# Performance work log

Measured on AMD Instinct MI355X. Metric: run time of the kernel, lower is better.

The kernel has to match this reference:

```python
import jax, jax.numpy as jnp
import numpy as np
import jax.lax as lax

B, S, E, H = 8, 4096, 1024, 128
TAU = 1.0
MIN_K = 32

def setup_inputs() -> dict:
    key = jax.random.key(0)
    k0, k1, k2, k3 = jax.random.split(key, 4)
    token_embeddings = jax.random.normal(k0, (B, S, E), dtype=jnp.float32)
    w1 = jax.random.normal(k1, (E, H), dtype=jnp.float32) * (1.0 / np.sqrt(E))
    b1 = jnp.zeros((H,), dtype=jnp.float32)
    w2 = jax.random.normal(k2, (H, 1), dtype=jnp.float32) * (1.0 / np.sqrt(H))
    b2 = jnp.zeros((1,), dtype=jnp.float32)
    # uniform noise for Gumbel, same bounds as the original module
    u = jax.random.uniform(k3, (B, S), minval=1e-08, maxval=1.0 - 1e-08, dtype=jnp.float32)
    return {"token_embeddings": token_embeddings, "w1": w1, "b1": b1, "w2": w2, "b2": b2, "u": u}

def reference(token_embeddings, w1, b1, w2, b2, u):
    # scorer MLP: Dense(H) -> relu -> Dense(1), squeeze -> [B, S]
    h = jax.nn.relu(jnp.einsum('bse,eh->bsh', token_embeddings, w1) + b1)
    importance_logits = (jnp.einsum('bsh,ho->bso', h, w2) + b2)[..., 0]  # [B, S]

    # expected_k (value_function is None): soft count of kept tokens
    expected_k = jax.nn.sigmoid(importance_logits).sum(axis=-1)  # [B]
    k = jnp.clip(expected_k.astype(jnp.int32), MIN_K, None)      # [B]

    # Gumbel-softmax top-k, hard=True
    gumbel = -jnp.log(-jnp.log(u))
    soft_mask = jax.nn.softmax((importance_logits + gumbel) / TAU, axis=-1)  # [B, S]

    # hard mask: 1.0 at the top-k[i] positions of soft_mask per row.
    # Equivalent to the original argsort + while_loop scatter: positions with
    # descending-sort rank < k[i] get 1.0.
    order = jnp.argsort(-soft_mask, axis=-1)          # [B, S] descending order
    ranks = jnp.argsort(order, axis=-1)               # rank of each position
    hard_mask = (ranks < k[:, None]).astype(soft_mask.dtype)

    selection_mask = lax.stop_gradient(hard_mask - soft_mask) + soft_mask
    filtered_embeddings = token_embeddings * selection_mask[..., None]
    return filtered_embeddings, selection_mask, expected_k
```

## Files before the change

kernel.cpp:

```cpp
#include <hip/hip_runtime.h>
#include <hip/hip_bf16.h>
#include <math.h>

#define B_ 8
#define S_ 4096
#define E_ 1024
#define H_ 128
#define MIN_K 32
#define OUT_MASK_OFF (B_*S_*E_)
#define OUT_EK_OFF   (B_*S_*E_ + B_*S_)

#define LOGITS_OFF 0
#define SOFT_OFF   131072
#define CNT_OFF    262144
#define KROW_OFF   393216
#define WB_OFF     393248

typedef __attribute__((ext_vector_type(8))) short   frag8;
typedef __attribute__((ext_vector_type(4))) float   fragc;

static __device__ __forceinline__ unsigned short bf16_rne(float f) {
  unsigned u = __float_as_uint(f);
  unsigned r = u + 0x7FFF + ((u >> 16) & 1);
  return (unsigned short)(r >> 16);
}
static __device__ __forceinline__ float bf16_to_f32(unsigned short h) {
  return __uint_as_float(((unsigned)h) << 16);
}

__global__ __launch_bounds__(256) void prep_w_kernel(
    const float* __restrict__ w1, unsigned short* __restrict__ wb)
{
  int id = blockIdx.x * 256 + threadIdx.x;
  int k  = id >> 5;
  int n4 = id & 31;
  float4 w = *(const float4*)(w1 + k * H_ + n4 * 4);
  int t  = k >> 5;
  int kp = k & 31;
#pragma unroll
  for (int e = 0; e < 4; ++e) {
    float f = (e == 0) ? w.x : (e == 1) ? w.y : (e == 2) ? w.z : w.w;
    unsigned short hi = bf16_rne(f);
    unsigned short lo = bf16_rne(f - bf16_to_f32(hi));
    int n = n4 * 4 + e;
    wb[t * 8192 +        n * 32 + kp] = hi;
    wb[t * 8192 + 4096 + n * 32 + kp] = lo;
  }
}

#define KT 32
#define NTILES (E_ / KT)
#define XS 40

__global__ __launch_bounds__(512, 2) void scorer_kernel(
    const float* __restrict__ x,
    const unsigned short* __restrict__ wb,
    const float* __restrict__ b1, const float* __restrict__ w2,
    const float* __restrict__ b2, float* __restrict__ logits)
{
  __shared__ unsigned short as_hi[2][128 * XS];
  __shared__ unsigned short as_lo[2][128 * XS];
  __shared__ unsigned short bs_hi[2][128 * XS];
  __shared__ unsigned short bs_lo[2][128 * XS];
  __shared__ float part[2][128];

  const int tid  = threadIdx.x;
  const int wv   = tid >> 6;
  const int lane = tid & 63;
  const int l15  = lane & 15;
  const int quad = lane >> 4;
  const int mg   = wv >> 1;
  const int ng   = wv & 1;
  const int m0   = blockIdx.x * 128;

  const int r = tid >> 2, p = tid & 3;
  const float* __restrict__ xsrc = x + (size_t)(m0 + r) * E_ + p * 8;
  const unsigned short* __restrict__ bsrc = wb + tid * 16;
  const int bplane = tid >> 8;
  const int boff   = ((tid >> 1) & 127) * XS + (tid & 1) * 16;
  const int aoff   = r * XS + p * 8;

  fragc acc[2][4];
#pragma unroll
  for (int mt = 0; mt < 2; ++mt)
#pragma unroll
    for (int nt = 0; nt < 4; ++nt)
      acc[mt][nt] = (fragc)(0.f);

  float4 a0 = *(const float4*)(xsrc);
  float4 a1 = *(const float4*)(xsrc + 4);
  uint4  q0 = *(const uint4*)(bsrc);
  uint4  q1 = *(const uint4*)(bsrc + 8);
  {
    frag8 h8, l8;
    float f[8] = {a0.x, a0.y, a0.z, a0.w, a1.x, a1.y, a1.z, a1.w};
#pragma unroll
    for (int e = 0; e < 8; ++e) {
      unsigned short hi = bf16_rne(f[e]);
      h8[e] = (short)hi; l8[e] = (short)bf16_rne(f[e] - bf16_to_f32(hi));
    }
    *(frag8*)&as_hi[0][aoff] = h8;
    *(frag8*)&as_lo[0][aoff] = l8;
    unsigned short* bd = bplane ? &bs_lo[0][boff] : &bs_hi[0][boff];
    *(uint4*)(bd) = q0;
    *(uint4*)(bd + 8) = q1;
  }
  __syncthreads();

#pragma unroll 1
  for (int t = 0; t < NTILES; ++t) {
    const int buf = t & 1;
    const bool more = (t + 1 < NTILES);

    float4 na0, na1; uint4 nq0, nq1;
    if (more) {
      na0 = *(const float4*)(xsrc + (t + 1) * KT);
      na1 = *(const float4*)(xsrc + (t + 1) * KT + 4);
      nq0 = *(const uint4*)(bsrc + (t + 1) * 8192);
      nq1 = *(const uint4*)(bsrc + (t + 1) * 8192 + 8);
    }

    frag8 ah[2], al[2], bh[4], bl[4];
#pragma unroll
    for (int mt = 0; mt < 2; ++mt) {
      int a = (mg * 32 + mt * 16 + l15) * XS + quad * 8;
      ah[mt] = *(const frag8*)&as_hi[buf][a];
      al[mt] = *(const frag8*)&as_lo[buf][a];
    }
#pragma unroll
    for (int nt = 0; nt < 4; ++nt) {
      int a = (ng * 64 + nt * 16 + l15) * XS + quad * 8;
      bh[nt] = *(const frag8*)&bs_hi[buf][a];
      bl[nt] = *(const frag8*)&bs_lo[buf][a];
    }

#pragma unroll
    for (int mt = 0; mt < 2; ++mt)
#pragma unroll
      for (int nt = 0; nt < 4; ++nt) {
        acc[mt][nt] = __builtin_amdgcn_mfma_f32_16x16x32_bf16(ah[mt], bh[nt], acc[mt][nt], 0, 0, 0);
        acc[mt][nt] = __builtin_amdgcn_mfma_f32_16x16x32_bf16(ah[mt], bl[nt], acc[mt][nt], 0, 0, 0);
        acc[mt][nt] = __builtin_amdgcn_mfma_f32_16x16x32_bf16(al[mt], bh[nt], acc[mt][nt], 0, 0, 0);
      }

    if (more) {
      frag8 h8, l8;
      float f[8] = {na0.x, na0.y, na0.z, na0.w, na1.x, na1.y, na1.z, na1.w};
#pragma unroll
      for (int e = 0; e < 8; ++e) {
        unsigned short hi = bf16_rne(f[e]);
        h8[e] = (short)hi; l8[e] = (short)bf16_rne(f[e] - bf16_to_f32(hi));
      }
      *(frag8*)&as_hi[buf ^ 1][aoff] = h8;
      *(frag8*)&as_lo[buf ^ 1][aoff] = l8;
      unsigned short* bd = bplane ? &bs_lo[buf ^ 1][boff] : &bs_hi[buf ^ 1][boff];
      *(uint4*)(bd) = nq0;
      *(uint4*)(bd + 8) = nq1;
    }
    __syncthreads();
  }

  float b1v[4], w2v[4];
#pragma unroll
  for (int nt = 0; nt < 4; ++nt) {
    int n = ng * 64 + nt * 16 + l15;
    b1v[nt] = b1[n]; w2v[nt] = w2[n];
  }
  float v[2][4];
#pragma unroll
  for (int mt = 0; mt < 2; ++mt)
#pragma unroll
    for (int reg = 0; reg < 4; ++reg) {
      float pacc = 0.f;
#pragma unroll
      for (int nt = 0; nt < 4; ++nt) {
        float h = acc[mt][nt][reg] + b1v[nt];
        h = h > 0.f ? h : 0.f;
        pacc = fmaf(h, w2v[nt], pacc);
      }
      v[mt][reg] = pacc;
    }
#pragma unroll
  for (int mask = 1; mask < 16; mask <<= 1)
#pragma unroll
    for (int mt = 0; mt < 2; ++mt)
#pragma unroll
      for (int reg = 0; reg < 4; ++reg)
        v[mt][reg] += __shfl_xor(v[mt][reg], mask);

  if (l15 == 0) {
#pragma unroll
    for (int mt = 0; mt < 2; ++mt)
#pragma unroll
      for (int reg = 0; reg < 4; ++reg)
        part[ng][mg * 32 + mt * 16 + quad * 4 + reg] = v[mt][reg];
  }
  __syncthreads();
  if (tid < 128)
    logits[m0 + tid] = (part[0][tid] + part[1][tid]) + b2[0];
}

__global__ __launch_bounds__(1024) void row_kernel(
    const float* __restrict__ logits, const float* __restrict__ u,
    float* __restrict__ soft, int* __restrict__ krow, float* __restrict__ ek_out)
{
  const int b = blockIdx.x;
  const int t = threadIdx.x;
  const float* Lrow = logits + b * S_;
  const float* urow = u + b * S_;

  __shared__ double red[1024];
  __shared__ float  redf[1024];

  float z[4];
  double psig = 0.0;
  float zmax = -INFINITY;
#pragma unroll
  for (int i = 0; i < 4; ++i) {
    int j = t + i * 1024;
    float L = Lrow[j];
    float g = -logf(-logf(urow[j]));
    z[i] = L + g;
    psig += (double)(1.f / (1.f + expf(-L)));
    zmax = fmaxf(zmax, z[i]);
  }
  red[t] = psig; redf[t] = zmax;
  __syncthreads();
  for (int s2 = 512; s2 > 0; s2 >>= 1) {
    if (t < s2) { red[t] += red[t + s2]; redf[t] = fmaxf(redf[t], redf[t + s2]); }
    __syncthreads();
  }
  __shared__ float m_sh; __shared__ double ek_sh;
  if (t == 0) { m_sh = redf[0]; ek_sh = red[0]; }
  __syncthreads();
  float m = m_sh;

  float e[4];
  double pexp = 0.0;
#pragma unroll
  for (int i = 0; i < 4; ++i) { e[i] = expf(z[i] - m); pexp += (double)e[i]; }
  red[t] = pexp;
  __syncthreads();
  for (int s2 = 512; s2 > 0; s2 >>= 1) {
    if (t < s2) red[t] += red[t + s2];
    __syncthreads();
  }
  __shared__ float den_sh;
  if (t == 0) den_sh = (float)red[0];
  __syncthreads();
  float den = den_sh;
#pragma unroll
  for (int i = 0; i < 4; ++i) soft[b * S_ + t + i * 1024] = e[i] / den;

  if (t == 0) {
    float ekf = (float)ek_sh;
    int k = (int)ekf;
    if (k < MIN_K) k = MIN_K;
    krow[b] = k;
    ek_out[b] = ekf;
  }
}

__global__ __launch_bounds__(256) void rank_kernel(
    const float* __restrict__ soft, int* __restrict__ counts)
{
  __shared__ float4 sjs[256];
  const int b  = blockIdx.z;
  const int ic = blockIdx.x;
  const int jc = blockIdx.y;
  const int tid = threadIdx.x;
  const float* row = soft + b * S_;

  sjs[tid] = ((const float4*)row)[jc * 256 + tid];
  const int i = ic * 256 + tid;
  const float si = row[i];
  __syncthreads();

  int cnt = 0;
  const int jbase = jc * 1024;
  for (int j4 = 0; j4 < 256; ++j4) {
    float4 vv = sjs[j4];
    int j = jbase + j4 * 4;
    cnt += (vv.x > si) || (vv.x == si && (j + 0) < i);
    cnt += (vv.y > si) || (vv.y == si && (j + 1) < i);
    cnt += (vv.z > si) || (vv.z == si && (j + 2) < i);
    cnt += (vv.w > si) || (vv.w == si && (j + 3) < i);
  }
  atomicAdd(&counts[b * S_ + i], cnt);
}

__global__ __launch_bounds__(256) void filter_kernel(
    const float* __restrict__ x, const float* __restrict__ soft,
    const int* __restrict__ counts, const int* __restrict__ krow,
    float* __restrict__ out, float* __restrict__ mask_out)
{
  const int token = blockIdx.x;
  const int b = token >> 12;
  const float s = soft[token];
  const float h = (counts[token] < krow[b]) ? 1.f : 0.f;
  const float sel = (h - s) + s;

  size_t base = (size_t)token * (E_ / 4) + threadIdx.x;
  float4 v = ((const float4*)x)[base];
  v.x *= sel; v.y *= sel; v.z *= sel; v.w *= sel;
  ((float4*)out)[base] = v;
  if (threadIdx.x == 0) mask_out[token] = sel;
}

extern "C" void kernel_launch(void* const* d_in, const int* in_sizes, int n_in,
                              void* d_out, int out_size, void* d_ws, size_t ws_size,
                              hipStream_t stream) {
  const float* x  = (const float*)d_in[0];
  const float* w1 = (const float*)d_in[1];
  const float* b1 = (const float*)d_in[2];
  const float* w2 = (const float*)d_in[3];
  const float* b2 = (const float*)d_in[4];
  const float* u  = (const float*)d_in[5];

  float* out = (float*)d_out;
  float* out_filt = out;
  float* out_mask = out + OUT_MASK_OFF;
  float* out_ek   = out + OUT_EK_OFF;

  char* ws = (char*)d_ws;
  float*          ws_logits = (float*)(ws + LOGITS_OFF);
  float*          ws_soft   = (float*)(ws + SOFT_OFF);
  int*            ws_cnt    = (int*)(ws + CNT_OFF);
  int*            ws_krow   = (int*)(ws + KROW_OFF);
  unsigned short* ws_wb     = (unsigned short*)(ws + WB_OFF);

  hipMemsetAsync(ws_cnt, 0, B_ * S_ * sizeof(int), stream);
  prep_w_kernel<<<dim3(128), dim3(256), 0, stream>>>(w1, ws_wb);
  scorer_kernel<<<dim3(B_ * S_ / 128), dim3(512), 0, stream>>>(
      x, ws_wb, b1, w2, b2, ws_logits);
  row_kernel<<<dim3(B_), dim3(1024), 0, stream>>>(ws_logits, u, ws_soft, ws_krow, out_ek);
  rank_kernel<<<dim3(16, 4, 8), dim3(256), 0, stream>>>(ws_soft, ws_cnt);
  filter_kernel<<<dim3(B_ * S_), dim3(256), 0, stream>>>(
      x, ws_soft, ws_cnt, ws_krow, out_filt, out_mask);
}
```

Before: 313.8 us.

## Stage raw fp32 activations in LDS and deepen global prefetch to two tiles

The scorer GEMM loop now stores raw fp32 activation tiles in shared memory and does the bf16 hi/lo split at fragment-load time, not before the LDS store. The loop is unrolled by two with register double-buffering, so global loads run two K-tiles ahead, and sched_barriers keep the loads issued before compute. This aims to hide global memory latency better and shorten the store path. In exchange, the split conversion is now repeated per wave that reads the same A rows (both N-groups), and register pressure rises from holding two prefetch stages.

```diff
diff --git a/kernel.cpp b/kernel.cpp
--- a/kernel.cpp
+++ b/kernel.cpp
@@ -50,7 +50,43 @@
 
 #define KT 32
 #define NTILES (E_ / KT)
+#define AS 36
 #define XS 40
+
+#define ISSUE_LOADS(Sa0, Sa1, Sq0, Sq1, T)                  \
+    Sa0 = *(const float4*)(xsrc + (T) * KT);                \
+    Sa1 = *(const float4*)(xsrc + (T) * KT + 4);            \
+    Sq0 = *(const uint4*)(bsrc + (T) * 8192);               \
+    Sq1 = *(const uint4*)(bsrc + (T) * 8192 + 8);
+
+#define WRITE_STAGE(BUF, Sa0, Sa1, Sq0, Sq1) {              \
+    *(float4*)&as_f[BUF][aoff]     = Sa0;                   \
+    *(float4*)&as_f[BUF][aoff + 4] = Sa1;                   \
+    unsigned short* bd_ = bplane ? &bs_lo[BUF][boff]        \
+                                 : &bs_hi[BUF][boff];       \
+    *(uint4*)(bd_)     = Sq0;                               \
+    *(uint4*)(bd_ + 8) = Sq1; }
+
+#define COMPUTE(BUF) {                                                        \
+    frag8 ah[2], al[2], bh[4], bl[4];                                         \
+    _Pragma("unroll") for (int mt = 0; mt < 2; ++mt) {                        \
+      int a_ = (mg * 32 + mt * 16 + l15) * AS + quad * 8;                     \
+      float4 f0_ = *(const float4*)&as_f[BUF][a_];                            \
+      float4 f1_ = *(const float4*)&as_f[BUF][a_ + 4];                        \
+      float ff_[8] = {f0_.x, f0_.y, f0_.z, f0_.w, f1_.x, f1_.y, f1_.z, f1_.w};\
+      _Pragma("unroll") for (int e = 0; e < 8; ++e) {                         \
+        unsigned short hi_ = bf16_rne(ff_[e]);                                \
+        ah[mt][e] = (short)hi_;                                               \
+        al[mt][e] = (short)bf16_rne(ff_[e] - bf16_to_f32(hi_)); } }           \
+    _Pragma("unroll") for (int nt = 0; nt < 4; ++nt) {                        \
+      int a_ = (ng * 64 + nt * 16 + l15) * XS + quad * 8;                     \
+      bh[nt] = *(const frag8*)&bs_hi[BUF][a_];                                \
+      bl[nt] = *(const frag8*)&bs_lo[BUF][a_]; }                              \
+    _Pragma("unroll") for (int mt = 0; mt < 2; ++mt)                          \
+      _Pragma("unroll") for (int nt = 0; nt < 4; ++nt) {                      \
+        acc[mt][nt] = __builtin_amdgcn_mfma_f32_16x16x32_bf16(ah[mt], bh[nt], acc[mt][nt], 0, 0, 0); \
+        acc[mt][nt] = __builtin_amdgcn_mfma_f32_16x16x32_bf16(ah[mt], bl[nt], acc[mt][nt], 0, 0, 0); \
+        acc[mt][nt] = __builtin_amdgcn_mfma_f32_16x16x32_bf16(al[mt], bh[nt], acc[mt][nt], 0, 0, 0); } }
 
 __global__ __launch_bounds__(512, 2) void scorer_kernel(
     const float* __restrict__ x,
@@ -58,8 +94,7 @@
     const float* __restrict__ b1, const float* __restrict__ w2,
     const float* __restrict__ b2, float* __restrict__ logits)
 {
-  __shared__ unsigned short as_hi[2][128 * XS];
-  __shared__ unsigned short as_lo[2][128 * XS];
+  __shared__ float          as_f[2][128 * AS];
   __shared__ unsigned short bs_hi[2][128 * XS];
   __shared__ unsigned short bs_lo[2][128 * XS];
   __shared__ float part[2][128];
@@ -78,7 +113,7 @@
   const unsigned short* __restrict__ bsrc = wb + tid * 16;
   const int bplane = tid >> 8;
   const int boff   = ((tid >> 1) & 127) * XS + (tid & 1) * 16;
-  const int aoff   = r * XS + p * 8;
+  const int aoff   = r * AS + p * 8;
 
   fragc acc[2][4];
 #pragma unroll
@@ -87,76 +122,25 @@
     for (int nt = 0; nt < 4; ++nt)
       acc[mt][nt] = (fragc)(0.f);
 
-  float4 a0 = *(const float4*)(xsrc);
-  float4 a1 = *(const float4*)(xsrc + 4);
-  uint4  q0 = *(const uint4*)(bsrc);
-  uint4  q1 = *(const uint4*)(bsrc + 8);
-  {
-    frag8 h8, l8;
-    float f[8] = {a0.x, a0.y, a0.z, a0.w, a1.x, a1.y, a1.z, a1.w};
-#pragma unroll
-    for (int e = 0; e < 8; ++e) {
-      unsigned short hi = bf16_rne(f[e]);
-      h8[e] = (short)hi; l8[e] = (short)bf16_rne(f[e] - bf16_to_f32(hi));
-    }
-    *(frag8*)&as_hi[0][aoff] = h8;
-    *(frag8*)&as_lo[0][aoff] = l8;
-    unsigned short* bd = bplane ? &bs_lo[0][boff] : &bs_hi[0][boff];
-    *(uint4*)(bd) = q0;
-    *(uint4*)(bd + 8) = q1;
-  }
-  __syncthreads();
-
-#pragma unroll 1
-  for (int t = 0; t < NTILES; ++t) {
-    const int buf = t & 1;
-    const bool more = (t + 1 < NTILES);
-
-    float4 na0, na1; uint4 nq0, nq1;
-    if (more) {
-      na0 = *(const float4*)(xsrc + (t + 1) * KT);
-      na1 = *(const float4*)(xsrc + (t + 1) * KT + 4);
-      nq0 = *(const uint4*)(bsrc + (t + 1) * 8192);
-      nq1 = *(const uint4*)(bsrc + (t + 1) * 8192 + 8);
-    }
-
-    frag8 ah[2], al[2], bh[4], bl[4];
-#pragma unroll
-    for (int mt = 0; mt < 2; ++mt) {
-      int a = (mg * 32 + mt * 16 + l15) * XS + quad * 8;
-      ah[mt] = *(const frag8*)&as_hi[buf][a];
-      al[mt] = *(const frag8*)&as_lo[buf][a];
-    }
-#pragma unroll
-    for (int nt = 0; nt < 4; ++nt) {
-      int a = (ng * 64 + nt * 16 + l15) * XS + quad * 8;
-      bh[nt] = *(const frag8*)&bs_hi[buf][a];
-      bl[nt] = *(const frag8*)&bs_lo[buf][a];
-    }
-
-#pragma unroll
-    for (int mt = 0; mt < 2; ++mt)
-#pragma unroll
-      for (int nt = 0; nt < 4; ++nt) {
-        acc[mt][nt] = __builtin_amdgcn_mfma_f32_16x16x32_bf16(ah[mt], bh[nt], acc[mt][nt], 0, 0, 0);
-        acc[mt][nt] = __builtin_amdgcn_mfma_f32_16x16x32_bf16(ah[mt], bl[nt], acc[mt][nt], 0, 0, 0);
-        acc[mt][nt] = __builtin_amdgcn_mfma_f32_16x16x32_bf16(al[mt], bh[nt], acc[mt][nt], 0, 0, 0);
-      }
-
-    if (more) {
-      frag8 h8, l8;
-      float f[8] = {na0.x, na0.y, na0.z, na0.w, na1.x, na1.y, na1.z, na1.w};
-#pragma unroll
-      for (int e = 0; e < 8; ++e) {
-        unsigned short hi = bf16_rne(f[e]);
-        h8[e] = (short)hi; l8[e] = (short)bf16_rne(f[e] - bf16_to_f32(hi));
-      }
-      *(frag8*)&as_hi[buf ^ 1][aoff] = h8;
-      *(frag8*)&as_lo[buf ^ 1][aoff] = l8;
-      unsigned short* bd = bplane ? &bs_lo[buf ^ 1][boff] : &bs_hi[buf ^ 1][boff];
-      *(uint4*)(bd) = nq0;
-      *(uint4*)(bd + 8) = nq1;
-    }
+  float4 a0_S0, a1_S0; uint4 q0_S0, q1_S0;
+  float4 a0_S1, a1_S1; uint4 q0_S1, q1_S1;
+
+  ISSUE_LOADS(a0_S0, a1_S0, q0_S0, q1_S0, 0)
+  ISSUE_LOADS(a0_S1, a1_S1, q0_S1, q1_S1, 1)
+  WRITE_STAGE(0, a0_S0, a1_S0, q0_S0, q1_S0)
+  __syncthreads();
+
+  for (int tp = 0; tp < 16; ++tp) {
+    const bool more = (tp < 15);
+    if (more) { ISSUE_LOADS(a0_S0, a1_S0, q0_S0, q1_S0, 2 * tp + 2) }
+    __builtin_amdgcn_sched_barrier(0);
+    COMPUTE(0)
+    WRITE_STAGE(1, a0_S1, a1_S1, q0_S1, q1_S1)
+    __syncthreads();
+    if (more) { ISSUE_LOADS(a0_S1, a1_S1, q0_S1, q1_S1, 2 * tp + 3) }
+    __builtin_amdgcn_sched_barrier(0);
+    COMPUTE(1)
+    if (more) { WRITE_STAGE(0, a0_S0, a1_S0, q0_S0, q1_S0) }
     __syncthreads();
   }
 
```

Result: no change. 311.6 us (-0.7%).

## Load scorer GEMM operands directly into registers with split-K across waves

Applied to the files above, without the earlier changes.

The scorer GEMM no longer stages A and B tiles through double-buffered shared memory. Each wave now reads x rows and pre-split bf16 weights straight from global memory into MFMA fragments. K is split across two wave halves, which are combined through a shared-memory reduction at the end, and each block covers 64 rows with 256 threads. This removes the per-tile LDS writes and barriers, at the cost of fragment-shaped (less coalesced) global loads, each wave re-converting x to hi/lo itself, more accumulator registers, and no explicit prefetch.

```diff
diff --git a/kernel.cpp b/kernel.cpp
--- a/kernel.cpp
+++ b/kernel.cpp
@@ -49,154 +49,138 @@
 }
 
 #define KT 32
-#define NTILES (E_ / KT)
-#define XS 40
-
-__global__ __launch_bounds__(512, 2) void scorer_kernel(
+#define RS 66
+
+__global__ __launch_bounds__(256, 2) void scorer_kernel(
     const float* __restrict__ x,
     const unsigned short* __restrict__ wb,
     const float* __restrict__ b1, const float* __restrict__ w2,
     const float* __restrict__ b2, float* __restrict__ logits)
 {
-  __shared__ unsigned short as_hi[2][128 * XS];
-  __shared__ unsigned short as_lo[2][128 * XS];
-  __shared__ unsigned short bs_hi[2][128 * XS];
-  __shared__ unsigned short bs_lo[2][128 * XS];
-  __shared__ float part[2][128];
+  __shared__ float red[2 * 64 * RS];
+  __shared__ float part[2][64];
 
   const int tid  = threadIdx.x;
   const int wv   = tid >> 6;
   const int lane = tid & 63;
   const int l15  = lane & 15;
   const int quad = lane >> 4;
-  const int mg   = wv >> 1;
-  const int ng   = wv & 1;
-  const int m0   = blockIdx.x * 128;
-
-  const int r = tid >> 2, p = tid & 3;
-  const float* __restrict__ xsrc = x + (size_t)(m0 + r) * E_ + p * 8;
-  const unsigned short* __restrict__ bsrc = wb + tid * 16;
-  const int bplane = tid >> 8;
-  const int boff   = ((tid >> 1) & 127) * XS + (tid & 1) * 16;
-  const int aoff   = r * XS + p * 8;
-
-  fragc acc[2][4];
-#pragma unroll
-  for (int mt = 0; mt < 2; ++mt)
+  const int kh   = wv & 1;
+  const int ng   = wv >> 1;
+  const int m0   = blockIdx.x * 64;
+
+  const float* __restrict__ ar0 = x + (size_t)(m0 + 0  + l15) * E_ + kh * 512 + quad * 8;
+  const float* __restrict__ ar1 = x + (size_t)(m0 + 16 + l15) * E_ + kh * 512 + quad * 8;
+  const float* __restrict__ ar2 = x + (size_t)(m0 + 32 + l15) * E_ + kh * 512 + quad * 8;
+  const float* __restrict__ ar3 = x + (size_t)(m0 + 48 + l15) * E_ + kh * 512 + quad * 8;
+
+  const unsigned short* __restrict__ bb =
+      wb + (size_t)kh * 16 * 8192 + (ng * 64 + l15) * 32 + quad * 8;
+
+  fragc acc[4][4];
+#pragma unroll
+  for (int mt = 0; mt < 4; ++mt)
 #pragma unroll
     for (int nt = 0; nt < 4; ++nt)
       acc[mt][nt] = (fragc)(0.f);
 
-  float4 a0 = *(const float4*)(xsrc);
-  float4 a1 = *(const float4*)(xsrc + 4);
-  uint4  q0 = *(const uint4*)(bsrc);
-  uint4  q1 = *(const uint4*)(bsrc + 8);
-  {
-    frag8 h8, l8;
-    float f[8] = {a0.x, a0.y, a0.z, a0.w, a1.x, a1.y, a1.z, a1.w};
-#pragma unroll
-    for (int e = 0; e < 8; ++e) {
-      unsigned short hi = bf16_rne(f[e]);
-      h8[e] = (short)hi; l8[e] = (short)bf16_rne(f[e] - bf16_to_f32(hi));
+#pragma unroll 2
+  for (int t = 0; t < 16; ++t) {
+    const int ko = t * KT;
+    frag8 ah[4], al[4];
+    {
+      const float* ars[4] = {ar0, ar1, ar2, ar3};
+#pragma unroll
+      for (int mt = 0; mt < 4; ++mt) {
+        float4 f0 = *(const float4*)(ars[mt] + ko);
+        float4 f1 = *(const float4*)(ars[mt] + ko + 4);
+        float ff[8] = {f0.x, f0.y, f0.z, f0.w, f1.x, f1.y, f1.z, f1.w};
+#pragma unroll
+        for (int e = 0; e < 8; ++e) {
+          unsigned short hi = bf16_rne(ff[e]);
+          ah[mt][e] = (short)hi;
+          al[mt][e] = (short)bf16_rne(ff[e] - bf16_to_f32(hi));
+        }
+      }
     }
-    *(frag8*)&as_hi[0][aoff] = h8;
-    *(frag8*)&as_lo[0][aoff] = l8;
-    unsigned short* bd = bplane ? &bs_lo[0][boff] : &bs_hi[0][boff];
-    *(uint4*)(bd) = q0;
-    *(uint4*)(bd + 8) = q1;
-  }
-  __syncthreads();
-
-#pragma unroll 1
-  for (int t = 0; t < NTILES; ++t) {
-    const int buf = t & 1;
-    const bool more = (t + 1 < NTILES);
-
-    float4 na0, na1; uint4 nq0, nq1;
-    if (more) {
-      na0 = *(const float4*)(xsrc + (t + 1) * KT);
-      na1 = *(const float4*)(xsrc + (t + 1) * KT + 4);
-      nq0 = *(const uint4*)(bsrc + (t + 1) * 8192);
-      nq1 = *(const uint4*)(bsrc + (t + 1) * 8192 + 8);
+    frag8 bh[4], bl[4];
+    {
+      const unsigned short* bt = bb + t * 8192;
+#pragma unroll
+      for (int nt = 0; nt < 4; ++nt) {
+        bh[nt] = *(const frag8*)(bt + nt * 512);
+        bl[nt] = *(const frag8*)(bt + 4096 + nt * 512);
+      }
     }
-
-    frag8 ah[2], al[2], bh[4], bl[4];
-#pragma unroll
-    for (int mt = 0; mt < 2; ++mt) {
-      int a = (mg * 32 + mt * 16 + l15) * XS + quad * 8;
-      ah[mt] = *(const frag8*)&as_hi[buf][a];
-      al[mt] = *(const frag8*)&as_lo[buf][a];
-    }
-#pragma unroll
-    for (int nt = 0; nt < 4; ++nt) {
-      int a = (ng * 64 + nt * 16 + l15) * XS + quad * 8;
-      bh[nt] = *(const frag8*)&bs_hi[buf][a];
-      bl[nt] = *(const frag8*)&bs_lo[buf][a];
-    }
-
-#pragma unroll
-    for (int mt = 0; mt < 2; ++mt)
+#pragma unroll
+    for (int mt = 0; mt < 4; ++mt)
 #pragma unroll
       for (int nt = 0; nt < 4; ++nt) {
         acc[mt][nt] = __builtin_amdgcn_mfma_f32_16x16x32_bf16(ah[mt], bh[nt], acc[mt][nt], 0, 0, 0);
         acc[mt][nt] = __builtin_amdgcn_mfma_f32_16x16x32_bf16(ah[mt], bl[nt], acc[mt][nt], 0, 0, 0);
         acc[mt][nt] = __builtin_amdgcn_mfma_f32_16x16x32_bf16(al[mt], bh[nt], acc[mt][nt], 0, 0, 0);
       }
-
-    if (more) {
-      frag8 h8, l8;
-      float f[8] = {na0.x, na0.y, na0.z, na0.w, na1.x, na1.y, na1.z, na1.w};
-#pragma unroll
-      for (int e = 0; e < 8; ++e) {
-        unsigned short hi = bf16_rne(f[e]);
-        h8[e] = (short)hi; l8[e] = (short)bf16_rne(f[e] - bf16_to_f32(hi));
+  }
+
+  const int rbase = (ng * 64 + lane) * RS;
+  if (kh == 1) {
+#pragma unroll
+    for (int mt = 0; mt < 4; ++mt)
+#pragma unroll
+      for (int nt = 0; nt < 4; ++nt)
+#pragma unroll
+        for (int reg = 0; reg < 4; ++reg)
+          red[rbase + mt * 16 + nt * 4 + reg] = acc[mt][nt][reg];
+  }
+  __syncthreads();
+
+  if (kh == 0) {
+#pragma unroll
+    for (int mt = 0; mt < 4; ++mt)
+#pragma unroll
+      for (int nt = 0; nt < 4; ++nt)
+#pragma unroll
+        for (int reg = 0; reg < 4; ++reg)
+          acc[mt][nt][reg] += red[rbase + mt * 16 + nt * 4 + reg];
+
+    float b1v[4], w2v[4];
+#pragma unroll
+    for (int nt = 0; nt < 4; ++nt) {
+      int n = ng * 64 + nt * 16 + l15;
+      b1v[nt] = b1[n]; w2v[nt] = w2[n];
+    }
+    float v[4][4];
+#pragma unroll
+    for (int mt = 0; mt < 4; ++mt)
+#pragma unroll
+      for (int reg = 0; reg < 4; ++reg) {
+        float pacc = 0.f;
+#pragma unroll
+        for (int nt = 0; nt < 4; ++nt) {
+          float h = acc[mt][nt][reg] + b1v[nt];
+          h = h > 0.f ? h : 0.f;
+          pacc = fmaf(h, w2v[nt], pacc);
+        }
+        v[mt][reg] = pacc;
       }
-      *(frag8*)&as_hi[buf ^ 1][aoff] = h8;
-      *(frag8*)&as_lo[buf ^ 1][aoff] = l8;
-      unsigned short* bd = bplane ? &bs_lo[buf ^ 1][boff] : &bs_hi[buf ^ 1][boff];
-      *(uint4*)(bd) = nq0;
-      *(uint4*)(bd + 8) = nq1;
+#pragma unroll
+    for (int mask = 1; mask < 16; mask <<= 1)
+#pragma unroll
+      for (int mt = 0; mt < 4; ++mt)
+#pragma unroll
+        for (int reg = 0; reg < 4; ++reg)
+          v[mt][reg] += __shfl_xor(v[mt][reg], mask);
+
+    if (l15 == 0) {
+#pragma unroll
+      for (int mt = 0; mt < 4; ++mt)
+#pragma unroll
+        for (int reg = 0; reg < 4; ++reg)
+          part[ng][mt * 16 + quad * 4 + reg] = v[mt][reg];
     }
-    __syncthreads();
-  }
-
-  float b1v[4], w2v[4];
-#pragma unroll
-  for (int nt = 0; nt < 4; ++nt) {
-    int n = ng * 64 + nt * 16 + l15;
-    b1v[nt] = b1[n]; w2v[nt] = w2[n];
-  }
-  float v[2][4];
-#pragma unroll
-  for (int mt = 0; mt < 2; ++mt)
-#pragma unroll
-    for (int reg = 0; reg < 4; ++reg) {
-      float pacc = 0.f;
-#pragma unroll
-      for (int nt = 0; nt < 4; ++nt) {
-        float h = acc[mt][nt][reg] + b1v[nt];
-        h = h > 0.f ? h : 0.f;
-        pacc = fmaf(h, w2v[nt], pacc);
-      }
-      v[mt][reg] = pacc;
-    }
-#pragma unroll
-  for (int mask = 1; mask < 16; mask <<= 1)
-#pragma unroll
-    for (int mt = 0; mt < 2; ++mt)
-#pragma unroll
-      for (int reg = 0; reg < 4; ++reg)
-        v[mt][reg] += __shfl_xor(v[mt][reg], mask);
-
-  if (l15 == 0) {
-#pragma unroll
-    for (int mt = 0; mt < 2; ++mt)
-#pragma unroll
-      for (int reg = 0; reg < 4; ++reg)
-        part[ng][mg * 32 + mt * 16 + quad * 4 + reg] = v[mt][reg];
-  }
-  __syncthreads();
-  if (tid < 128)
+  }
+  __syncthreads();
+  if (tid < 64)
     logits[m0 + tid] = (part[0][tid] + part[1][tid]) + b2[0];
 }
 
@@ -331,7 +315,7 @@
 
   hipMemsetAsync(ws_cnt, 0, B_ * S_ * sizeof(int), stream);
   prep_w_kernel<<<dim3(128), dim3(256), 0, stream>>>(w1, ws_wb);
-  scorer_kernel<<<dim3(B_ * S_ / 128), dim3(512), 0, stream>>>(
+  scorer_kernel<<<dim3(B_ * S_ / 64), dim3(256), 0, stream>>>(
       x, ws_wb, b1, w2, b2, ws_logits);
   row_kernel<<<dim3(B_), dim3(1024), 0, stream>>>(ws_logits, u, ws_soft, ws_krow, out_ek);
   rank_kernel<<<dim3(16, 4, 8), dim3(256), 0, stream>>>(ws_soft, ws_cnt);
```

Measured after the change: 314.3 us. About the same (+0.2%).
